# Kernel tuning notes

Measured on AMD Instinct MI355X. Metric: run time of the kernel, lower is better.

Reference implementation:

```python
import math
import jax, jax.numpy as jnp
import numpy as np

HIDDEN = 1024

def setup_inputs() -> dict:
    key = jax.random.key(0)
    kx, kq, kk, kv = jax.random.split(key, 4)
    scale = 1.0 / math.sqrt(HIDDEN)
    x = jax.random.normal(kx, (4, 2048, HIDDEN), dtype=jnp.float32)
    # nn.Linear weights, stored as [out, in] like torch; y = x @ W.T
    Wq = jax.random.normal(kq, (HIDDEN, HIDDEN), dtype=jnp.float32) * scale
    Wk = jax.random.normal(kk, (HIDDEN, HIDDEN), dtype=jnp.float32) * scale
    Wv = jax.random.normal(kv, (HIDDEN, HIDDEN), dtype=jnp.float32) * scale
    return {"x": x, "Wq": Wq, "Wk": Wk, "Wv": Wv}

def reference(x, Wq, Wk, Wv):
    # Q,K,V: [b, s, d]
    Q = jnp.einsum('bsd,ed->bse', x, Wq)
    K = jnp.einsum('bsd,ed->bse', x, Wk)
    V = jnp.einsum('bsd,ed->bse', x, Wv)
    scores = jnp.einsum('bqd,bkd->bqk', Q, K) / math.sqrt(x.shape[-1])
    att = jax.nn.softmax(scores, axis=-1)  # stable max-subtracted softmax, same math as _softmax
    return jnp.einsum('bqk,bkd->bqd', att, V)
```

## Files before the change

kernel.cpp:

```cpp
#include <hip/hip_runtime.h>
#include <stdint.h>

typedef unsigned int uint;
typedef unsigned short ushort;
typedef __attribute__((ext_vector_type(8))) short short8;
typedef __attribute__((ext_vector_type(4))) float floatx4;

__device__ inline ushort f2b(float f) {
  union { float f; uint u; } c; c.f = f;
  uint u = c.u;
  u = (u + 0x7fffu + ((u >> 16) & 1u)) >> 16;
  return (ushort)u;
}

__device__ inline void gl_lds16(const ushort* g, ushort* l) {
  __builtin_amdgcn_global_load_lds(
      (const __attribute__((address_space(1))) void*)g,
      (__attribute__((address_space(3))) void*)l, 16, 0, 0);
}

__global__ __launch_bounds__(256) void cvt_all(
    const float* __restrict__ x,  const float* __restrict__ wq,
    const float* __restrict__ wk, const float* __restrict__ wv,
    ushort* __restrict__ xb, ushort* __restrict__ wb)
{
  const int b = blockIdx.x;
  const float* s; ushort* d; int i;
  if (b < 4096) {
    s = x; d = xb; i = b * 256 + threadIdx.x;
  } else {
    int t = b - 4096;
    int wsel = t >> 9;
    s = (wsel == 0) ? wq : (wsel == 1) ? wk : wv;
    d = wb + (size_t)wsel * (1024u * 1024u);
    i = (t & 511) * 256 + threadIdx.x;
  }
  float4 a = ((const float4*)s)[i * 2];
  float4 c = ((const float4*)s)[i * 2 + 1];
  short8 v;
  v[0] = (short)f2b(a.x); v[1] = (short)f2b(a.y);
  v[2] = (short)f2b(a.z); v[3] = (short)f2b(a.w);
  v[4] = (short)f2b(c.x); v[5] = (short)f2b(c.y);
  v[6] = (short)f2b(c.z); v[7] = (short)f2b(c.w);
  ((short8*)d)[i] = v;
}

template <int MODE>
__global__ __launch_bounds__(256) void gemm_bt(
    const ushort* __restrict__ A, int lda, size_t sA,
    const ushort* __restrict__ B, int ldb, size_t sB,
    void* __restrict__ C, int ldc, size_t sC,
    int K, float scale)
{
  __shared__ ushort As[128 * 64];
  __shared__ ushort Bs[128 * 64];

  const int tid = threadIdx.x;
  const int bz  = blockIdx.z;
  A += (size_t)bz * sA;
  B += (size_t)bz * sB;

  const int m0 = blockIdx.y * 128;
  const int n0 = blockIdx.x * 128;

  const int lane = tid & 63;
  const int w    = tid >> 6;
  const int l16  = lane & 15;
  const int quad = lane >> 4;
  const int mw   = w >> 1;
  const int nw   = w & 1;

  const ushort* agp[4];
  const ushort* bgp[4];
#pragma unroll
  for (int c4 = 0; c4 < 4; ++c4) {
    int r   = c4 * 32 + (tid >> 3);
    int sw  = (r ^ (r >> 3)) & 7;
    int col = ((tid & 7) ^ sw) * 8;
    agp[c4] = A + (size_t)(m0 + r) * lda + col;
    bgp[c4] = B + (size_t)(n0 + r) * ldb + col;
  }

  int aoff[4], boff[4];
#pragma unroll
  for (int i = 0; i < 4; ++i) {
    int ra = mw * 64 + i * 16 + l16;
    aoff[i] = ra * 64 + ((quad ^ ((ra ^ (ra >> 3)) & 7)) * 8);
    int rb = nw * 64 + i * 16 + l16;
    boff[i] = rb * 64 + ((quad ^ ((rb ^ (rb >> 3)) & 7)) * 8);
  }

  floatx4 acc[4][4];
#pragma unroll
  for (int i = 0; i < 4; ++i)
#pragma unroll
    for (int j = 0; j < 4; ++j)
#pragma unroll
      for (int r = 0; r < 4; ++r) acc[i][j][r] = 0.f;

  for (int k0 = 0; k0 < K; k0 += 64) {
    __syncthreads();
#pragma unroll
    for (int c4 = 0; c4 < 4; ++c4) {
      gl_lds16(agp[c4], &As[(c4 * 32 + w * 8) * 64]);
      gl_lds16(bgp[c4], &Bs[(c4 * 32 + w * 8) * 64]);
      agp[c4] += 64; bgp[c4] += 64;
    }
    __syncthreads();

#pragma unroll
    for (int h = 0; h < 2; ++h) {
      short8 af[4], bf[4];
#pragma unroll
      for (int i = 0; i < 4; ++i) {
        af[i] = *(const short8*)&As[aoff[i] ^ (h * 32)];
        bf[i] = *(const short8*)&Bs[boff[i] ^ (h * 32)];
      }
#pragma unroll
      for (int i = 0; i < 4; ++i)
#pragma unroll
        for (int j = 0; j < 4; ++j)
          acc[i][j] = __builtin_amdgcn_mfma_f32_16x16x32_bf16(
              af[i], bf[j], acc[i][j], 0, 0, 0);
    }
  }

#pragma unroll
  for (int i = 0; i < 4; ++i)
#pragma unroll
    for (int j = 0; j < 4; ++j) {
      const int mg = m0 + mw * 64 + i * 16 + quad * 4;
      const int ng = n0 + nw * 64 + j * 16 + l16;
      if (MODE == 2 || MODE == 3) {
        float* Cb = (float*)C + (size_t)bz * sC;
#pragma unroll
        for (int r = 0; r < 4; ++r)
          Cb[(size_t)(mg + r) * ldc + ng] =
              (MODE == 2) ? acc[i][j][r] * scale : acc[i][j][r];
      } else {
        ushort* Qo = (ushort*)C;
        if (ng < 2048) {
          ushort* dst = Qo + (size_t)(ng >> 10) * (8192u * 1024u);
          const int nn = ng & 1023;
#pragma unroll
          for (int r = 0; r < 4; ++r)
            dst[(size_t)(mg + r) * 1024 + nn] = f2b(acc[i][j][r]);
        } else {
          ushort* Vo = Qo + (size_t)2 * 8192 * 1024;
          uint lo = (uint)f2b(acc[i][j][0]) | ((uint)f2b(acc[i][j][1]) << 16);
          uint hi = (uint)f2b(acc[i][j][2]) | ((uint)f2b(acc[i][j][3]) << 16);
          *(uint2*)&Vo[(size_t)(ng - 2048) * 8192 + mg] = make_uint2(lo, hi);
        }
      }
    }
}

__global__ __launch_bounds__(256) void softmax_row(float* __restrict__ S) {
  __shared__ float red[8];
  const int t = threadIdx.x;
  const int w = t >> 6;
  float* row = S + (size_t)blockIdx.x * 2048;

  float4 v0 = *(const float4*)(row + t * 8);
  float4 v1 = *(const float4*)(row + t * 8 + 4);
  float v[8] = {v0.x, v0.y, v0.z, v0.w, v1.x, v1.y, v1.z, v1.w};

  float mx = v[0];
#pragma unroll
  for (int i = 1; i < 8; ++i) mx = fmaxf(mx, v[i]);
#pragma unroll
  for (int d = 1; d < 64; d <<= 1) mx = fmaxf(mx, __shfl_xor(mx, d));
  if ((t & 63) == 0) red[w] = mx;
  __syncthreads();
  mx = fmaxf(fmaxf(red[0], red[1]), fmaxf(red[2], red[3]));

  float p[8], sum = 0.f;
#pragma unroll
  for (int i = 0; i < 8; ++i) { p[i] = exp2f(v[i] - mx); sum += p[i]; }
#pragma unroll
  for (int d = 1; d < 64; d <<= 1) sum += __shfl_xor(sum, d);
  if ((t & 63) == 0) red[4 + w] = sum;
  __syncthreads();
  const float inv = 1.0f / (red[4] + red[5] + red[6] + red[7]);

  short8 o;
#pragma unroll
  for (int i = 0; i < 8; ++i) o[i] = (short)f2b(p[i] * inv);
  *(short8*)((ushort*)row + t * 8) = o;
}

extern "C" void kernel_launch(void* const* d_in, const int* in_sizes, int n_in,
                              void* d_out, int out_size, void* d_ws, size_t ws_size,
                              hipStream_t stream) {
  const float* x  = (const float*)d_in[0];
  const float* Wq = (const float*)d_in[1];
  const float* Wk = (const float*)d_in[2];
  const float* Wv = (const float*)d_in[3];
  float* outp = (float*)d_out;

  const float SCALE = 1.4426950408889634f / 32.0f;

  const size_t NEED_1B   = 90177536;
  const size_t NEED_FULL = 140509184;

  ushort* xb = (ushort*)d_ws;
  ushort* Wb = xb + (size_t)8192 * 1024;
  ushort* Qb = Wb + (size_t)3 * 1024 * 1024;
  ushort* Kb = Qb + (size_t)8192 * 1024;
  ushort* Vt = Kb + (size_t)8192 * 1024;
  float*  S  = (float*)(Vt + (size_t)8192 * 1024);

  cvt_all<<<5632, 256, 0, stream>>>(x, Wq, Wk, Wv, xb, Wb);

  gemm_bt<4><<<dim3(24, 64, 1), 256, 0, stream>>>(
      xb, 1024, 0, Wb, 1024, 0, Qb, 0, 0, 1024, 1.f);

  if (ws_size >= NEED_FULL) {
    gemm_bt<2><<<dim3(16, 16, 4), 256, 0, stream>>>(
        Qb, 1024, (size_t)2048 * 1024, Kb, 1024, (size_t)2048 * 1024,
        S, 2048, (size_t)2048 * 2048, 1024, SCALE);
    softmax_row<<<8192, 256, 0, stream>>>(S);
    gemm_bt<3><<<dim3(8, 16, 4), 256, 0, stream>>>(
        (const ushort*)S, 4096, (size_t)2048 * 4096, Vt, 8192, 2048,
        outp, 1024, (size_t)2048 * 1024, 2048, 1.f);
  } else {
    for (int b = 0; b < 4; ++b) {
      gemm_bt<2><<<dim3(16, 16, 1), 256, 0, stream>>>(
          Qb + (size_t)b * 2048 * 1024, 1024, 0,
          Kb + (size_t)b * 2048 * 1024, 1024, 0,
          S, 2048, 0, 1024, SCALE);
      softmax_row<<<2048, 256, 0, stream>>>(S);
      gemm_bt<3><<<dim3(8, 16, 1), 256, 0, stream>>>(
          (const ushort*)S, 4096, 0, Vt + (size_t)b * 2048, 8192, 0,
          outp + (size_t)b * 2048 * 1024, 1024, 0, 2048, 1.f);
    }
  }
}
```

Before: 261.5 us.

## Use 32x32x16 MFMA tiles and store attention scores as bf16

The GEMM inner loop moves from a 4x4 grid of 16x16x32 bf16 MFMAs to a 2x2 grid of 32x32x16 MFMAs per wave, with reworked LDS fragment addressing and epilogue indexing. This cuts the number of LDS fragment loads per MFMA. The score matrix is now written as bf16 instead of fp32, which halves the traffic for score writes and for the softmax read. The softmax then overwrites the same bf16 buffer in place, so the workspace need shrinks. In exchange the unnormalised scores are rounded to bf16 before the softmax, which costs some accuracy.

```diff
diff --git a/kernel.cpp b/kernel.cpp
--- a/kernel.cpp
+++ b/kernel.cpp
@@ -4,13 +4,16 @@
 typedef unsigned int uint;
 typedef unsigned short ushort;
 typedef __attribute__((ext_vector_type(8))) short short8;
-typedef __attribute__((ext_vector_type(4))) float floatx4;
+typedef __attribute__((ext_vector_type(16))) float floatx16;
 
 __device__ inline ushort f2b(float f) {
   union { float f; uint u; } c; c.f = f;
   uint u = c.u;
   u = (u + 0x7fffu + ((u >> 16) & 1u)) >> 16;
   return (ushort)u;
+}
+__device__ inline float b2f(ushort u) {
+  union { uint i; float f; } c; c.i = ((uint)u) << 16; return c.f;
 }
 
 __device__ inline void gl_lds16(const ushort* g, ushort* l) {
@@ -65,8 +68,8 @@
 
   const int lane = tid & 63;
   const int w    = tid >> 6;
-  const int l16  = lane & 15;
-  const int quad = lane >> 4;
+  const int l32  = lane & 31;
+  const int lh   = lane >> 5;
   const int mw   = w >> 1;
   const int nw   = w & 1;
 
@@ -81,22 +84,22 @@
     bgp[c4] = B + (size_t)(n0 + r) * ldb + col;
   }
 
-  int aoff[4], boff[4];
-#pragma unroll
-  for (int i = 0; i < 4; ++i) {
-    int ra = mw * 64 + i * 16 + l16;
-    aoff[i] = ra * 64 + ((quad ^ ((ra ^ (ra >> 3)) & 7)) * 8);
-    int rb = nw * 64 + i * 16 + l16;
-    boff[i] = rb * 64 + ((quad ^ ((rb ^ (rb >> 3)) & 7)) * 8);
-  }
-
-  floatx4 acc[4][4];
-#pragma unroll
-  for (int i = 0; i < 4; ++i)
-#pragma unroll
-    for (int j = 0; j < 4; ++j)
-#pragma unroll
-      for (int r = 0; r < 4; ++r) acc[i][j][r] = 0.f;
+  int arow[2], brow[2], aswz[2], bswz[2];
+#pragma unroll
+  for (int t = 0; t < 2; ++t) {
+    arow[t] = mw * 64 + t * 32 + l32;
+    aswz[t] = (arow[t] ^ (arow[t] >> 3)) & 7;
+    brow[t] = nw * 64 + t * 32 + l32;
+    bswz[t] = (brow[t] ^ (brow[t] >> 3)) & 7;
+  }
+
+  floatx16 acc[2][2];
+#pragma unroll
+  for (int i = 0; i < 2; ++i)
+#pragma unroll
+    for (int j = 0; j < 2; ++j)
+#pragma unroll
+      for (int r = 0; r < 16; ++r) acc[i][j][r] = 0.f;
 
   for (int k0 = 0; k0 < K; k0 += 64) {
     __syncthreads();
@@ -109,61 +112,79 @@
     __syncthreads();
 
 #pragma unroll
-    for (int h = 0; h < 2; ++h) {
-      short8 af[4], bf[4];
-#pragma unroll
-      for (int i = 0; i < 4; ++i) {
-        af[i] = *(const short8*)&As[aoff[i] ^ (h * 32)];
-        bf[i] = *(const short8*)&Bs[boff[i] ^ (h * 32)];
+    for (int s = 0; s < 4; ++s) {
+      short8 af[2], bf[2];
+#pragma unroll
+      for (int t = 0; t < 2; ++t) {
+        af[t] = *(const short8*)&As[arow[t] * 64 + (((s * 2 + lh) ^ aswz[t]) * 8)];
+        bf[t] = *(const short8*)&Bs[brow[t] * 64 + (((s * 2 + lh) ^ bswz[t]) * 8)];
       }
 #pragma unroll
-      for (int i = 0; i < 4; ++i)
-#pragma unroll
-        for (int j = 0; j < 4; ++j)
-          acc[i][j] = __builtin_amdgcn_mfma_f32_16x16x32_bf16(
+      for (int i = 0; i < 2; ++i)
+#pragma unroll
+        for (int j = 0; j < 2; ++j)
+          acc[i][j] = __builtin_amdgcn_mfma_f32_32x32x16_bf16(
               af[i], bf[j], acc[i][j], 0, 0, 0);
     }
   }
 
 #pragma unroll
-  for (int i = 0; i < 4; ++i)
-#pragma unroll
-    for (int j = 0; j < 4; ++j) {
-      const int mg = m0 + mw * 64 + i * 16 + quad * 4;
-      const int ng = n0 + nw * 64 + j * 16 + l16;
-      if (MODE == 2 || MODE == 3) {
+  for (int i = 0; i < 2; ++i)
+#pragma unroll
+    for (int j = 0; j < 2; ++j) {
+      const int mbase = m0 + mw * 64 + i * 32 + 4 * lh;
+      const int ng    = n0 + nw * 64 + j * 32 + l32;
+      if (MODE == 2) {
         float* Cb = (float*)C + (size_t)bz * sC;
 #pragma unroll
-        for (int r = 0; r < 4; ++r)
-          Cb[(size_t)(mg + r) * ldc + ng] =
-              (MODE == 2) ? acc[i][j][r] * scale : acc[i][j][r];
+        for (int g = 0; g < 4; ++g)
+#pragma unroll
+          for (int r = 0; r < 4; ++r)
+            Cb[(size_t)(mbase + 8 * g + r) * ldc + ng] = acc[i][j][4 * g + r];
+      } else if (MODE == 1) {
+        ushort* Cb = (ushort*)C + (size_t)bz * sC;
+#pragma unroll
+        for (int g = 0; g < 4; ++g)
+#pragma unroll
+          for (int r = 0; r < 4; ++r)
+            Cb[(size_t)(mbase + 8 * g + r) * ldc + ng] =
+                f2b(acc[i][j][4 * g + r] * scale);
       } else {
-        ushort* Qo = (ushort*)C;
         if (ng < 2048) {
-          ushort* dst = Qo + (size_t)(ng >> 10) * (8192u * 1024u);
+          ushort* dst = (ushort*)C + (size_t)(ng >> 10) * (8192u * 1024u);
           const int nn = ng & 1023;
 #pragma unroll
-          for (int r = 0; r < 4; ++r)
-            dst[(size_t)(mg + r) * 1024 + nn] = f2b(acc[i][j][r]);
+          for (int g = 0; g < 4; ++g)
+#pragma unroll
+            for (int r = 0; r < 4; ++r)
+              dst[(size_t)(mbase + 8 * g + r) * 1024 + nn] =
+                  f2b(acc[i][j][4 * g + r]);
         } else {
-          ushort* Vo = Qo + (size_t)2 * 8192 * 1024;
-          uint lo = (uint)f2b(acc[i][j][0]) | ((uint)f2b(acc[i][j][1]) << 16);
-          uint hi = (uint)f2b(acc[i][j][2]) | ((uint)f2b(acc[i][j][3]) << 16);
-          *(uint2*)&Vo[(size_t)(ng - 2048) * 8192 + mg] = make_uint2(lo, hi);
+          ushort* Vo = (ushort*)C + (size_t)2 * 8192 * 1024;
+#pragma unroll
+          for (int g = 0; g < 4; ++g) {
+            uint lo = (uint)f2b(acc[i][j][4 * g + 0]) |
+                      ((uint)f2b(acc[i][j][4 * g + 1]) << 16);
+            uint hi = (uint)f2b(acc[i][j][4 * g + 2]) |
+                      ((uint)f2b(acc[i][j][4 * g + 3]) << 16);
+            *(uint2*)&Vo[(size_t)(ng - 2048) * 8192 + mbase + 8 * g] =
+                make_uint2(lo, hi);
+          }
         }
       }
     }
 }
 
-__global__ __launch_bounds__(256) void softmax_row(float* __restrict__ S) {
+__global__ __launch_bounds__(256) void softmax_row(ushort* __restrict__ S) {
   __shared__ float red[8];
   const int t = threadIdx.x;
   const int w = t >> 6;
-  float* row = S + (size_t)blockIdx.x * 2048;
-
-  float4 v0 = *(const float4*)(row + t * 8);
-  float4 v1 = *(const float4*)(row + t * 8 + 4);
-  float v[8] = {v0.x, v0.y, v0.z, v0.w, v1.x, v1.y, v1.z, v1.w};
+  ushort* row = S + (size_t)blockIdx.x * 2048;
+
+  short8 raw = ((const short8*)row)[t];
+  float v[8];
+#pragma unroll
+  for (int i = 0; i < 8; ++i) v[i] = b2f((ushort)raw[i]);
 
   float mx = v[0];
 #pragma unroll
@@ -186,7 +207,7 @@
   short8 o;
 #pragma unroll
   for (int i = 0; i < 8; ++i) o[i] = (short)f2b(p[i] * inv);
-  *(short8*)((ushort*)row + t * 8) = o;
+  ((short8*)row)[t] = o;
 }
 
 extern "C" void kernel_launch(void* const* d_in, const int* in_sizes, int n_in,
@@ -200,38 +221,38 @@
 
   const float SCALE = 1.4426950408889634f / 32.0f;
 
-  const size_t NEED_1B   = 90177536;
-  const size_t NEED_FULL = 140509184;
-
   ushort* xb = (ushort*)d_ws;
   ushort* Wb = xb + (size_t)8192 * 1024;
   ushort* Qb = Wb + (size_t)3 * 1024 * 1024;
   ushort* Kb = Qb + (size_t)8192 * 1024;
   ushort* Vt = Kb + (size_t)8192 * 1024;
-  float*  S  = (float*)(Vt + (size_t)8192 * 1024);
+  ushort* Sb = Vt + (size_t)8192 * 1024;
+
+  const size_t NEED_FULL = 106954752;
+  const size_t NEED_1B   = 81788928;
 
   cvt_all<<<5632, 256, 0, stream>>>(x, Wq, Wk, Wv, xb, Wb);
 
-  gemm_bt<4><<<dim3(24, 64, 1), 256, 0, stream>>>(
+  gemm_bt<0><<<dim3(24, 64, 1), 256, 0, stream>>>(
       xb, 1024, 0, Wb, 1024, 0, Qb, 0, 0, 1024, 1.f);
 
   if (ws_size >= NEED_FULL) {
-    gemm_bt<2><<<dim3(16, 16, 4), 256, 0, stream>>>(
+    gemm_bt<1><<<dim3(16, 16, 4), 256, 0, stream>>>(
         Qb, 1024, (size_t)2048 * 1024, Kb, 1024, (size_t)2048 * 1024,
-        S, 2048, (size_t)2048 * 2048, 1024, SCALE);
-    softmax_row<<<8192, 256, 0, stream>>>(S);
-    gemm_bt<3><<<dim3(8, 16, 4), 256, 0, stream>>>(
-        (const ushort*)S, 4096, (size_t)2048 * 4096, Vt, 8192, 2048,
+        Sb, 2048, (size_t)2048 * 2048, 1024, SCALE);
+    softmax_row<<<8192, 256, 0, stream>>>(Sb);
+    gemm_bt<2><<<dim3(8, 16, 4), 256, 0, stream>>>(
+        Sb, 2048, (size_t)2048 * 2048, Vt, 8192, 2048,
         outp, 1024, (size_t)2048 * 1024, 2048, 1.f);
   } else {
     for (int b = 0; b < 4; ++b) {
-      gemm_bt<2><<<dim3(16, 16, 1), 256, 0, stream>>>(
+      gemm_bt<1><<<dim3(16, 16, 1), 256, 0, stream>>>(
           Qb + (size_t)b * 2048 * 1024, 1024, 0,
           Kb + (size_t)b * 2048 * 1024, 1024, 0,
-          S, 2048, 0, 1024, SCALE);
-      softmax_row<<<2048, 256, 0, stream>>>(S);
-      gemm_bt<3><<<dim3(8, 16, 1), 256, 0, stream>>>(
-          (const ushort*)S, 4096, 0, Vt + (size_t)b * 2048, 8192, 0,
+          Sb, 2048, 0, 1024, SCALE);
+      softmax_row<<<2048, 256, 0, stream>>>(Sb);
+      gemm_bt<2><<<dim3(8, 16, 1), 256, 0, stream>>>(
+          Sb, 2048, 0, Vt + (size_t)b * 2048, 8192, 0,
           outp + (size_t)b * 2048 * 1024, 1024, 0, 2048, 1.f);
     }
   }
```

New measurement: 261.8 us. About the same (+0.1%).
